# Kernel tuning notes

Hardware: AMD Instinct MI355X
Metric: run time of the kernel (lower is better)

## Reference

```python
import jax, jax.numpy as jnp
import numpy as np

H = 2048            # hidden_size
IN = 64             # input_size
EMB = 8             # EMBEDDING_DIMS
LIN = IN - 4 + 4 * EMB  # 92, LSTM input width
NH = 13             # number of prediction heads
MAXO = 9            # max head output width (gear)
HEAD_OUTS = [5, 1, 1, 1, 1, 1, 1, 1, 9, 1, 3, 1, 1]
LN_EPS = 1e-5


def setup_inputs() -> dict:
    key = jax.random.key(0)
    ks = jax.random.split(key, 22)
    s = 1.0 / np.sqrt(H)
    d = {}
    d["lap_cont"] = jax.random.normal(ks[0], (1, 1, IN - 4), jnp.float32)
    d["idx"] = jax.random.randint(ks[1], (1, 1, 4), 0, 5)  # compound, driver, track, team
    d["h_s"] = 0.1 * jax.random.normal(ks[2], (2, 1, H), jnp.float32)
    d["c_s"] = 0.1 * jax.random.normal(ks[3], (2, 1, H), jnp.float32)
    d["emb_team"] = 0.02 * jax.random.normal(ks[4], (10, EMB), jnp.float32)
    d["emb_track"] = 0.02 * jax.random.normal(ks[5], (48, EMB), jnp.float32)
    d["emb_driver"] = 0.02 * jax.random.normal(ks[6], (46, EMB), jnp.float32)
    d["emb_compound"] = 0.02 * jax.random.normal(ks[7], (5, EMB), jnp.float32)
    d["W_ih0"] = s * jax.random.normal(ks[8], (4 * H, LIN), jnp.float32)
    d["W_hh0"] = s * jax.random.normal(ks[9], (4 * H, H), jnp.float32)
    d["b_ih0"] = s * jax.random.normal(ks[10], (4 * H,), jnp.float32)
    d["b_hh0"] = s * jax.random.normal(ks[11], (4 * H,), jnp.float32)
    d["W_ih1"] = s * jax.random.normal(ks[12], (4 * H, H), jnp.float32)
    d["W_hh1"] = s * jax.random.normal(ks[13], (4 * H, H), jnp.float32)
    d["b_ih1"] = s * jax.random.normal(ks[14], (4 * H,), jnp.float32)
    d["b_hh1"] = s * jax.random.normal(ks[15], (4 * H,), jnp.float32)
    d["ln_g"] = jnp.ones((H,), jnp.float32)
    d["ln_b"] = jnp.zeros((H,), jnp.float32)
    d["head_W1"] = 0.02 * jax.random.normal(ks[16], (NH, 64, H), jnp.float32)
    d["head_b1"] = 0.02 * jax.random.normal(ks[17], (NH, 64), jnp.float32)
    d["head_W2"] = 0.02 * jax.random.normal(ks[18], (NH, MAXO, 64), jnp.float32)  # padded to MAXO
    d["head_b2"] = 0.02 * jax.random.normal(ks[19], (NH, MAXO), jnp.float32)
    return d


def _lstm_cell(x, h, c, Wih, Whh, bih, bhh):
    # x:[1,in], h,c:[1,H]; PyTorch gate order i,f,g,o
    g = x @ Wih.T + bih + h @ Whh.T + bhh
    i, f, gg, o = jnp.split(g, 4, axis=-1)
    c_new = jax.nn.sigmoid(f) * c + jax.nn.sigmoid(i) * jnp.tanh(gg)
    h_new = jax.nn.sigmoid(o) * jnp.tanh(c_new)
    return h_new, c_new


def reference(lap_cont, idx, h_s, c_s, emb_team, emb_track, emb_driver, emb_compound,
              W_ih0, W_hh0, b_ih0, b_hh0, W_ih1, W_hh1, b_ih1, b_hh1,
              ln_g, ln_b, head_W1, head_b1, head_W2, head_b2):
    # Embeddings (idx order: compound, driver, track_status, team)
    comp_e = emb_compound[idx[:, :, 0]]
    drv_e = emb_driver[idx[:, :, 1]]
    trk_e = emb_track[idx[:, :, 2]]
    team_e = emb_team[idx[:, :, 3]]
    x = jnp.concatenate([lap_cont, team_e, trk_e, drv_e, comp_e], axis=-1)  # [1,1,LIN]

    x2 = x[0]  # seq_len=1 -> single cell step; [1,LIN]
    h0, c0 = _lstm_cell(x2, h_s[0], c_s[0], W_ih0, W_hh0, b_ih0, b_hh0)
    h1, c1 = _lstm_cell(h0, h_s[1], c_s[1], W_ih1, W_hh1, b_ih1, b_hh1)
    new_h = jnp.stack([h0, h1], axis=0)
    new_c = jnp.stack([c0, c1], axis=0)

    h_t = h1[None]  # [1,1,H]
    mu = jnp.mean(h_t, axis=-1, keepdims=True)
    var = jnp.mean(jnp.square(h_t - mu), axis=-1, keepdims=True)
    h_t = (h_t - mu) * jax.lax.rsqrt(var + LN_EPS) * ln_g + ln_b

    # All 13 heads fused: Dropout is identity at inference
    hid = jax.nn.relu(jnp.einsum('bsh,koh->bsko', h_t, head_W1) + head_b1)  # [1,1,13,64]
    outs = jnp.einsum('bsko,kpo->bskp', hid, head_W2) + head_b2              # [1,1,13,9]

    heads = [outs[:, :, k, :HEAD_OUTS[k]] for k in range(NH)]
    return (new_h, new_c, *heads)
```

## Files before the change

### kernel.cpp

```cpp
#include <hip/hip_runtime.h>

#define H 2048

__device__ __align__(16) float g_p1[4 * H];
__device__ __align__(16) float g_h0[H];
__device__ __align__(16) float g_h1[H];
__device__ __align__(16) float g_hid[13 * 64];

__device__ __forceinline__ float sg(float x) { return 1.f / (1.f + __expf(-x)); }

__device__ __forceinline__ float wred(float x) {
    #pragma unroll
    for (int o = 32; o > 0; o >>= 1) x += __shfl_down(x, o);
    return x;
}

__device__ __forceinline__ void gl_lds(const float* g, float* l) {
    __builtin_amdgcn_global_load_lds(
        (const __attribute__((address_space(1))) void*)g,
        (__attribute__((address_space(3))) void*)l,
        16, 0, 0);
}

__device__ __forceinline__ float dot_lds(const float* row, const float* vec, int lane) {
    float acc = 0.f;
    #pragma unroll
    for (int c = 0; c < 8; c++) {
        float4 a = *reinterpret_cast<const float4*>(row + c * 256 + lane * 4);
        float4 v = *reinterpret_cast<const float4*>(vec + c * 256 + lane * 4);
        acc = fmaf(a.x, v.x, acc); acc = fmaf(a.y, v.y, acc);
        acc = fmaf(a.z, v.z, acc); acc = fmaf(a.w, v.w, acc);
    }
    return acc;
}

__global__ __launch_bounds__(256) void k1(
    const float* __restrict__ lap, const int* __restrict__ idx,
    const float* __restrict__ h_s, const float* __restrict__ c_s,
    const float* __restrict__ e_team, const float* __restrict__ e_trk,
    const float* __restrict__ e_drv, const float* __restrict__ e_cmp,
    const float* __restrict__ Wih0, const float* __restrict__ Whh0,
    const float* __restrict__ bih0, const float* __restrict__ bhh0,
    const float* __restrict__ Whh1, const float* __restrict__ bih1,
    const float* __restrict__ bhh1, float* __restrict__ out)
{
    __shared__ float rows[4][H];
    __shared__ float vec[H];
    __shared__ float xsh[96];
    __shared__ float gsh[4];
    int tid = threadIdx.x, w = tid >> 6, lane = tid & 63;
    int b = blockIdx.x;
    bool l0 = b < 2048;

    long row = l0 ? (b + (long)w * H) : ((long)(b - 2048) * 4 + w);
    const float* rp  = (l0 ? Whh0 : Whh1) + row * H;
    const float* src = l0 ? h_s : (h_s + H);

    #pragma unroll
    for (int c = 0; c < 8; c++) gl_lds(rp + c * 256 + lane * 4, &rows[w][c * 256]);
    #pragma unroll
    for (int c = 0; c < 2; c++) {
        int cc = w * 2 + c;
        gl_lds(src + cc * 256 + lane * 4, &vec[cc * 256]);
    }

    float wv0 = 0.f, wv1 = 0.f;
    if (l0) {
        const float* wr = Wih0 + row * 92;
        wv0 = wr[lane];
        if (lane < 28) wv1 = wr[lane + 64];
        if (tid < 92) {
            float v;
            if (tid < 60)      v = lap[tid];
            else if (tid < 68) v = e_team[idx[3] * 8 + tid - 60];
            else if (tid < 76) v = e_trk [idx[2] * 8 + tid - 68];
            else if (tid < 84) v = e_drv [idx[1] * 8 + tid - 76];
            else               v = e_cmp [idx[0] * 8 + tid - 84];
            xsh[tid] = v;
        }
    }
    __syncthreads();

    float acc = dot_lds(rows[w], vec, lane);
    if (l0) {
        float p = xsh[lane] * wv0;
        if (lane < 28) p += xsh[lane + 64] * wv1;
        acc += p;
    }
    acc = wred(acc);

    if (l0) {
        if (lane == 0) gsh[w] = acc + bih0[row] + bhh0[row];
        __syncthreads();
        if (tid == 0) {
            int j = b;
            float gi = gsh[0], gf = gsh[1], gg = gsh[2], go = gsh[3];
            float cp = c_s[j];
            float cn = sg(gf) * cp + sg(gi) * tanhf(gg);
            float hn = sg(go) * tanhf(cn);
            out[j]         = hn;
            out[2 * H + j] = cn;
            g_h0[j] = hn;
        }
    } else {
        if (lane == 0) g_p1[row] = acc + bih1[row] + bhh1[row];
    }
}

__global__ __launch_bounds__(256) void k2(
    const float* __restrict__ Wih1, const float* __restrict__ c_s,
    float* __restrict__ out)
{
    __shared__ float rows[4][H];
    __shared__ float vec[H];
    __shared__ float gsh[4];
    int tid = threadIdx.x, w = tid >> 6, lane = tid & 63;
    int j = blockIdx.x;
    long row = j + (long)w * H;
    const float* rp = Wih1 + row * H;
    #pragma unroll
    for (int c = 0; c < 8; c++) gl_lds(rp + c * 256 + lane * 4, &rows[w][c * 256]);
    #pragma unroll
    for (int c = 0; c < 2; c++) {
        int cc = w * 2 + c;
        gl_lds(g_h0 + cc * 256 + lane * 4, &vec[cc * 256]);
    }
    __syncthreads();

    float acc = wred(dot_lds(rows[w], vec, lane));
    if (lane == 0) gsh[w] = acc + g_p1[row];
    __syncthreads();
    if (tid == 0) {
        float gi = gsh[0], gf = gsh[1], gg = gsh[2], go = gsh[3];
        float cp = c_s[H + j];
        float cn = sg(gf) * cp + sg(gi) * tanhf(gg);
        float hn = sg(go) * tanhf(cn);
        out[H + j]     = hn;
        out[3 * H + j] = cn;
        g_h1[j] = hn;
    }
}

__global__ __launch_bounds__(256) void k3(
    const float* __restrict__ ln_g, const float* __restrict__ ln_b,
    const float* __restrict__ W1, const float* __restrict__ b1)
{
    __shared__ float rows[4][H];
    __shared__ float ht[H];
    __shared__ float red[8];
    __shared__ float mvs[2];
    int tid = threadIdx.x, w = tid >> 6, lane = tid & 63;
    int k = blockIdx.x >> 4;
    int o = (blockIdx.x & 15) * 4 + w;
    const float* rp = W1 + ((long)k * 64 + o) * H;
    #pragma unroll
    for (int c = 0; c < 8; c++) gl_lds(rp + c * 256 + lane * 4, &rows[w][c * 256]);

    float v[8];
    float s = 0.f, s2 = 0.f;
    #pragma unroll
    for (int i = 0; i < 8; i++) {
        float x = g_h1[tid + i * 256];
        v[i] = x; s += x; s2 += x * x;
    }
    s = wred(s); s2 = wred(s2);
    if (lane == 0) { red[w] = s; red[4 + w] = s2; }
    __syncthreads();
    if (tid == 0) {
        float ts = red[0] + red[1] + red[2] + red[3];
        float t2 = red[4] + red[5] + red[6] + red[7];
        float mu = ts / (float)H;
        float var = t2 / (float)H - mu * mu;
        mvs[0] = mu; mvs[1] = rsqrtf(var + 1e-5f);
    }
    __syncthreads();
    float mu = mvs[0], rs = mvs[1];
    #pragma unroll
    for (int i = 0; i < 8; i++) {
        int e = tid + i * 256;
        ht[e] = (v[i] - mu) * rs * ln_g[e] + ln_b[e];
    }
    __syncthreads();

    float acc = wred(dot_lds(rows[w], ht, lane));
    if (lane == 0) {
        float r = acc + b1[k * 64 + o];
        g_hid[k * 64 + o] = r > 0.f ? r : 0.f;
    }
}

__global__ __launch_bounds__(128) void k4(
    const float* __restrict__ W2, const float* __restrict__ b2,
    float* __restrict__ out)
{
    const int HO[13]  = {5,1,1,1,1,1,1,1,9,1,3,1,1};
    const int OFF[13] = {0,5,6,7,8,9,10,11,12,21,22,25,26};
    int t = threadIdx.x;
    if (t >= 117) return;
    int k = t / 9, p = t % 9;
    if (p >= HO[k]) return;
    const float* wr = W2 + ((long)k * 9 + p) * 64;
    const float* hp = g_hid + k * 64;
    float acc = b2[k * 9 + p];
    #pragma unroll
    for (int o = 0; o < 64; o++) acc = fmaf(hp[o], wr[o], acc);
    out[4 * H + OFF[k] + p] = acc;
}

extern "C" void kernel_launch(void* const* d_in, const int* in_sizes, int n_in,
                              void* d_out, int out_size, void* d_ws, size_t ws_size,
                              hipStream_t stream) {
    const float* lap    = (const float*)d_in[0];
    const int*   idx    = (const int*)  d_in[1];
    const float* h_s    = (const float*)d_in[2];
    const float* c_s    = (const float*)d_in[3];
    const float* e_team = (const float*)d_in[4];
    const float* e_trk  = (const float*)d_in[5];
    const float* e_drv  = (const float*)d_in[6];
    const float* e_cmp  = (const float*)d_in[7];
    const float* Wih0   = (const float*)d_in[8];
    const float* Whh0   = (const float*)d_in[9];
    const float* bih0   = (const float*)d_in[10];
    const float* bhh0   = (const float*)d_in[11];
    const float* Wih1   = (const float*)d_in[12];
    const float* Whh1   = (const float*)d_in[13];
    const float* bih1   = (const float*)d_in[14];
    const float* bhh1   = (const float*)d_in[15];
    const float* ln_g   = (const float*)d_in[16];
    const float* ln_b   = (const float*)d_in[17];
    const float* hW1    = (const float*)d_in[18];
    const float* hb1    = (const float*)d_in[19];
    const float* hW2    = (const float*)d_in[20];
    const float* hb2    = (const float*)d_in[21];
    float* out = (float*)d_out;

    k1<<<4096, 256, 0, stream>>>(lap, idx, h_s, c_s, e_team, e_trk, e_drv, e_cmp,
                                 Wih0, Whh0, bih0, bhh0, Whh1, bih1, bhh1, out);
    k2<<<2048, 256, 0, stream>>>(Wih1, c_s, out);
    k3<<<208, 256, 0, stream>>>(ln_g, ln_b, hW1, hb1);
    k4<<<1, 128, 0, stream>>>(hW2, hb2, out);
}
```

Before: 252.2 us.

## Give each wave one hidden unit's gate rows with double-buffered LDS streaming

The LSTM gate kernels are reorganised so each wavefront owns one hidden unit and computes all four gate rows for it. In k1 that is eight rows: four from Whh0 and four from Whh1. The rows are streamed through a per-wave double-buffered LDS area using global_load_lds, with explicit vmcnt waits, so the next row's load overlaps the current dot product. The h vectors are held in registers instead of being staged in LDS, and block-level barriers and shared gate reductions are removed, so the grids shrink from 4096/2048 blocks to 512. The 64KB of LDS per block may limit occupancy and therefore memory parallelism, and correctness depends on the hand-encoded waitcnt values.

```diff
diff --git a/kernel.cpp b/kernel.cpp
--- a/kernel.cpp
+++ b/kernel.cpp
@@ -6,6 +6,9 @@
 __device__ __align__(16) float g_h0[H];
 __device__ __align__(16) float g_h1[H];
 __device__ __align__(16) float g_hid[13 * 64];
+
+#define WAIT_VM8 0xF78
+#define WAIT_VM0 0xF70
 
 __device__ __forceinline__ float sg(float x) { return 1.f / (1.f + __expf(-x)); }
 
@@ -20,18 +23,6 @@
         (const __attribute__((address_space(1))) void*)g,
         (__attribute__((address_space(3))) void*)l,
         16, 0, 0);
-}
-
-__device__ __forceinline__ float dot_lds(const float* row, const float* vec, int lane) {
-    float acc = 0.f;
-    #pragma unroll
-    for (int c = 0; c < 8; c++) {
-        float4 a = *reinterpret_cast<const float4*>(row + c * 256 + lane * 4);
-        float4 v = *reinterpret_cast<const float4*>(vec + c * 256 + lane * 4);
-        acc = fmaf(a.x, v.x, acc); acc = fmaf(a.y, v.y, acc);
-        acc = fmaf(a.z, v.z, acc); acc = fmaf(a.w, v.w, acc);
-    }
-    return acc;
 }
 
 __global__ __launch_bounds__(256) void k1(
@@ -44,66 +35,88 @@
     const float* __restrict__ Whh1, const float* __restrict__ bih1,
     const float* __restrict__ bhh1, float* __restrict__ out)
 {
-    __shared__ float rows[4][H];
-    __shared__ float vec[H];
-    __shared__ float xsh[96];
-    __shared__ float gsh[4];
+    __shared__ float buf[4][2][H];
     int tid = threadIdx.x, w = tid >> 6, lane = tid & 63;
-    int b = blockIdx.x;
-    bool l0 = b < 2048;
-
-    long row = l0 ? (b + (long)w * H) : ((long)(b - 2048) * 4 + w);
-    const float* rp  = (l0 ? Whh0 : Whh1) + row * H;
-    const float* src = l0 ? h_s : (h_s + H);
-
-    #pragma unroll
-    for (int c = 0; c < 8; c++) gl_lds(rp + c * 256 + lane * 4, &rows[w][c * 256]);
-    #pragma unroll
-    for (int c = 0; c < 2; c++) {
-        int cc = w * 2 + c;
-        gl_lds(src + cc * 256 + lane * 4, &vec[cc * 256]);
-    }
-
-    float wv0 = 0.f, wv1 = 0.f;
-    if (l0) {
-        const float* wr = Wih0 + row * 92;
-        wv0 = wr[lane];
-        if (lane < 28) wv1 = wr[lane + 64];
-        if (tid < 92) {
-            float v;
-            if (tid < 60)      v = lap[tid];
-            else if (tid < 68) v = e_team[idx[3] * 8 + tid - 60];
-            else if (tid < 76) v = e_trk [idx[2] * 8 + tid - 68];
-            else if (tid < 84) v = e_drv [idx[1] * 8 + tid - 76];
-            else               v = e_cmp [idx[0] * 8 + tid - 84];
-            xsh[tid] = v;
-        }
-    }
-    __syncthreads();
-
-    float acc = dot_lds(rows[w], vec, lane);
-    if (l0) {
-        float p = xsh[lane] * wv0;
-        if (lane < 28) p += xsh[lane + 64] * wv1;
-        acc += p;
-    }
-    acc = wred(acc);
-
-    if (l0) {
-        if (lane == 0) gsh[w] = acc + bih0[row] + bhh0[row];
-        __syncthreads();
-        if (tid == 0) {
-            int j = b;
-            float gi = gsh[0], gf = gsh[1], gg = gsh[2], go = gsh[3];
-            float cp = c_s[j];
-            float cn = sg(gf) * cp + sg(gi) * tanhf(gg);
-            float hn = sg(go) * tanhf(cn);
-            out[j]         = hn;
-            out[2 * H + j] = cn;
-            g_h0[j] = hn;
-        }
-    } else {
-        if (lane == 0) g_p1[row] = acc + bih1[row] + bhh1[row];
+    int wid = blockIdx.x * 4 + w;
+
+    float4 va[8], vb[8];
+    #pragma unroll
+    for (int c = 0; c < 8; c++) {
+        va[c] = *reinterpret_cast<const float4*>(h_s + c * 256 + lane * 4);
+        vb[c] = *reinterpret_cast<const float4*>(h_s + H + c * 256 + lane * 4);
+    }
+    float xa, xb = 0.f;
+    {
+        int i = lane;
+        xa = (i < 60) ? lap[i]
+           : (i < 68) ? e_team[idx[3] * 8 + i - 60]
+           : (i < 76) ? e_trk [idx[2] * 8 + i - 68]
+           : (i < 84) ? e_drv [idx[1] * 8 + i - 76]
+                      : e_cmp [idx[0] * 8 + i - 84];
+        if (lane < 28) {
+            int j2 = lane + 64;
+            xb = (j2 < 68) ? e_team[idx[3] * 8 + j2 - 60]
+               : (j2 < 76) ? e_trk [idx[2] * 8 + j2 - 68]
+               : (j2 < 84) ? e_drv [idx[1] * 8 + j2 - 76]
+                           : e_cmp [idx[0] * 8 + j2 - 84];
+        }
+    }
+
+    const float* rp[8];
+    #pragma unroll
+    for (int k = 0; k < 8; k++) {
+        const float* W = (k < 4) ? Whh0 : Whh1;
+        rp[k] = W + ((long)wid + (long)(k & 3) * H) * H;
+    }
+
+    #pragma unroll
+    for (int c = 0; c < 8; c++) gl_lds(rp[0] + c * 256 + lane * 4, &buf[w][0][c * 256]);
+
+    float dsum[8];
+    #pragma unroll
+    for (int k = 0; k < 8; k++) {
+        if (k < 7) {
+            #pragma unroll
+            for (int c = 0; c < 8; c++)
+                gl_lds(rp[k + 1] + c * 256 + lane * 4, &buf[w][(k + 1) & 1][c * 256]);
+            __builtin_amdgcn_s_waitcnt(WAIT_VM8);
+        } else {
+            __builtin_amdgcn_s_waitcnt(WAIT_VM0);
+        }
+        const float* r = buf[w][k & 1];
+        float acc = 0.f;
+        #pragma unroll
+        for (int c = 0; c < 8; c++) {
+            float4 a = *reinterpret_cast<const float4*>(r + c * 256 + lane * 4);
+            float4 v = (k < 4) ? va[c] : vb[c];
+            acc = fmaf(a.x, v.x, acc); acc = fmaf(a.y, v.y, acc);
+            acc = fmaf(a.z, v.z, acc); acc = fmaf(a.w, v.w, acc);
+        }
+        dsum[k] = acc;
+    }
+
+    float gate[4], p1v[4];
+    #pragma unroll
+    for (int g = 0; g < 4; g++) {
+        const float* wr = Wih0 + ((long)wid + (long)g * H) * 92;
+        float p = xa * wr[lane] + ((lane < 28) ? xb * wr[lane + 64] : 0.f);
+        gate[g] = wred(dsum[g] + p);
+        p1v[g]  = wred(dsum[4 + g]);
+    }
+    if (lane == 0) {
+        float gi = gate[0] + bih0[wid]         + bhh0[wid];
+        float gf = gate[1] + bih0[wid + H]     + bhh0[wid + H];
+        float gg = gate[2] + bih0[wid + 2 * H] + bhh0[wid + 2 * H];
+        float go = gate[3] + bih0[wid + 3 * H] + bhh0[wid + 3 * H];
+        float cp = c_s[wid];
+        float cn = sg(gf) * cp + sg(gi) * tanhf(gg);
+        float hn = sg(go) * tanhf(cn);
+        out[wid]         = hn;
+        out[2 * H + wid] = cn;
+        g_h0[wid] = hn;
+        #pragma unroll
+        for (int g = 0; g < 4; g++)
+            g_p1[wid + g * H] = p1v[g] + bih1[wid + g * H] + bhh1[wid + g * H];
     }
 }
 
@@ -111,33 +124,58 @@
     const float* __restrict__ Wih1, const float* __restrict__ c_s,
     float* __restrict__ out)
 {
-    __shared__ float rows[4][H];
-    __shared__ float vec[H];
-    __shared__ float gsh[4];
+    __shared__ float buf[4][2][H];
     int tid = threadIdx.x, w = tid >> 6, lane = tid & 63;
-    int j = blockIdx.x;
-    long row = j + (long)w * H;
-    const float* rp = Wih1 + row * H;
-    #pragma unroll
-    for (int c = 0; c < 8; c++) gl_lds(rp + c * 256 + lane * 4, &rows[w][c * 256]);
-    #pragma unroll
-    for (int c = 0; c < 2; c++) {
-        int cc = w * 2 + c;
-        gl_lds(g_h0 + cc * 256 + lane * 4, &vec[cc * 256]);
-    }
-    __syncthreads();
-
-    float acc = wred(dot_lds(rows[w], vec, lane));
-    if (lane == 0) gsh[w] = acc + g_p1[row];
-    __syncthreads();
-    if (tid == 0) {
-        float gi = gsh[0], gf = gsh[1], gg = gsh[2], go = gsh[3];
-        float cp = c_s[H + j];
+    int wid = blockIdx.x * 4 + w;
+
+    float4 va[8];
+    #pragma unroll
+    for (int c = 0; c < 8; c++)
+        va[c] = *reinterpret_cast<const float4*>(g_h0 + c * 256 + lane * 4);
+
+    const float* rp[4];
+    #pragma unroll
+    for (int k = 0; k < 4; k++)
+        rp[k] = Wih1 + ((long)wid + (long)k * H) * H;
+
+    #pragma unroll
+    for (int c = 0; c < 8; c++) gl_lds(rp[0] + c * 256 + lane * 4, &buf[w][0][c * 256]);
+
+    float dsum[4];
+    #pragma unroll
+    for (int k = 0; k < 4; k++) {
+        if (k < 3) {
+            #pragma unroll
+            for (int c = 0; c < 8; c++)
+                gl_lds(rp[k + 1] + c * 256 + lane * 4, &buf[w][(k + 1) & 1][c * 256]);
+            __builtin_amdgcn_s_waitcnt(WAIT_VM8);
+        } else {
+            __builtin_amdgcn_s_waitcnt(WAIT_VM0);
+        }
+        const float* r = buf[w][k & 1];
+        float acc = 0.f;
+        #pragma unroll
+        for (int c = 0; c < 8; c++) {
+            float4 a = *reinterpret_cast<const float4*>(r + c * 256 + lane * 4);
+            acc = fmaf(a.x, va[c].x, acc); acc = fmaf(a.y, va[c].y, acc);
+            acc = fmaf(a.z, va[c].z, acc); acc = fmaf(a.w, va[c].w, acc);
+        }
+        dsum[k] = acc;
+    }
+    float gate[4];
+    #pragma unroll
+    for (int k = 0; k < 4; k++) gate[k] = wred(dsum[k]);
+    if (lane == 0) {
+        float gi = gate[0] + g_p1[wid];
+        float gf = gate[1] + g_p1[wid + H];
+        float gg = gate[2] + g_p1[wid + 2 * H];
+        float go = gate[3] + g_p1[wid + 3 * H];
+        float cp = c_s[H + wid];
         float cn = sg(gf) * cp + sg(gi) * tanhf(gg);
         float hn = sg(go) * tanhf(cn);
-        out[H + j]     = hn;
-        out[3 * H + j] = cn;
-        g_h1[j] = hn;
+        out[H + wid]     = hn;
+        out[3 * H + wid] = cn;
+        g_h1[wid] = hn;
     }
 }
 
@@ -182,7 +220,15 @@
     }
     __syncthreads();
 
-    float acc = wred(dot_lds(rows[w], ht, lane));
+    float acc = 0.f;
+    #pragma unroll
+    for (int c = 0; c < 8; c++) {
+        float4 a = *reinterpret_cast<const float4*>(rows[w] + c * 256 + lane * 4);
+        float4 vv = *reinterpret_cast<const float4*>(ht + c * 256 + lane * 4);
+        acc = fmaf(a.x, vv.x, acc); acc = fmaf(a.y, vv.y, acc);
+        acc = fmaf(a.z, vv.z, acc); acc = fmaf(a.w, vv.w, acc);
+    }
+    acc = wred(acc);
     if (lane == 0) {
         float r = acc + b1[k * 64 + o];
         g_hid[k * 64 + o] = r > 0.f ? r : 0.f;
@@ -234,9 +280,9 @@
     const float* hb2    = (const float*)d_in[21];
     float* out = (float*)d_out;
 
-    k1<<<4096, 256, 0, stream>>>(lap, idx, h_s, c_s, e_team, e_trk, e_drv, e_cmp,
-                                 Wih0, Whh0, bih0, bhh0, Whh1, bih1, bhh1, out);
-    k2<<<2048, 256, 0, stream>>>(Wih1, c_s, out);
+    k1<<<512, 256, 0, stream>>>(lap, idx, h_s, c_s, e_team, e_trk, e_drv, e_cmp,
+                                Wih0, Whh0, bih0, bhh0, Whh1, bih1, bhh1, out);
+    k2<<<512, 256, 0, stream>>>(Wih1, c_s, out);
     k3<<<208, 256, 0, stream>>>(ln_g, ln_b, hW1, hb1);
     k4<<<1, 128, 0, stream>>>(hW2, hb2, out);
 }
```

Result: no change. 251.4 us (-0.3%).
